# Kernel tuning notes

Hardware: AMD Instinct MI355X
Metric: run time of the kernel (lower is better)

## Reference

```python
import jax, jax.numpy as jnp
import numpy as np
from jax import lax

R = 10          # 10 iterations of (3x3x3 conv > 0) == one binary box dilation of radius 10
TOP_N = 250
SMOOTH = 1e-5
WEIGHT_CE = 1.0
WEIGHT_DICE = 1.0
FR_WEIGHT = 5.0


def _box_dilate(mask, r=R):
    # binary dilation with a (2r+1)^3 box, done separably along D,H,W
    x = mask.astype(jnp.float32)
    for axis in (1, 2, 3):
        win = [1, 1, 1, 1]
        win[axis] = 2 * r + 1
        x = lax.reduce_window(x, 0.0, lax.max, tuple(win), (1, 1, 1, 1), 'SAME')
    return x > 0


def _masked_mean(x, mask):
    cnt = jnp.sum(mask)
    s = jnp.sum(jnp.where(mask, x, 0.0))
    return jnp.where(cnt > 0, s / jnp.maximum(cnt, 1), 0.0)


def _fr_loss(feature, label):
    pos = label[:, 0] == 1                                  # (B,D,H,W)
    neg = label[:, 0] == 0
    f = jnp.moveaxis(feature, 1, -1)                        # (B,D,H,W,C)
    cnt = jnp.sum(pos)
    # mean positive feature (zeros if no positives)
    mean_pos = jnp.sum(jnp.where(pos[..., None], f, 0.0), axis=(0, 1, 2, 3)) / jnp.maximum(cnt, 1)
    std_feat = jnp.where(cnt > 0, mean_pos, 0.0)
    std_n = std_feat / jnp.maximum(jnp.linalg.norm(std_feat), 1e-12)
    # normalized feature map; cosine of a normalized feature with std_n == dot product
    f_n = f / jnp.maximum(jnp.linalg.norm(f, axis=-1, keepdims=True), 1e-12)
    cos_map = jnp.einsum('bdhwc,c->bdhw', f_n, std_n)
    # 1) positive compactness loss
    positive_loss = _masked_mean(1.0 - cos_map, pos)
    easy = _box_dilate(pos) & (~pos)
    mis_loss = _masked_mean(jax.nn.relu(cos_map), easy)
    # 3) hardest negatives: top-250 negative similarities, scatter to mask, dilate
    neg_sims = jnp.where(neg, cos_map, -1e30).reshape(-1)
    top_v, top_i = lax.top_k(neg_sims, TOP_N)
    hi = jnp.zeros(neg_sims.shape, jnp.float32).at[top_i].set((top_v > -1e29).astype(jnp.float32))
    hi = hi.reshape(pos.shape) > 0
    final_neg = _box_dilate(hi) & (~pos)
    neg_loss = _masked_mean(jax.nn.relu(cos_map), final_neg)
    return positive_loss + mis_loss + neg_loss


def _ce_and_dice(net_output, target):
    C = net_output.shape[1]
    logp = jax.nn.log_softmax(net_output, axis=1)           # (B,C,D,H,W)
    ce = -jnp.mean(jnp.take_along_axis(logp, target, axis=1))
    p = jnp.exp(logp)
    y = jax.nn.one_hot(target[:, 0], C, dtype=p.dtype)      # (B,D,H,W,C)
    y = jnp.moveaxis(y, -1, 1)                               # (B,C,D,H,W)
    axes = (0, 2, 3, 4)                                      # batch_dice=True
    tp = jnp.sum(p * y, axes)
    fp = jnp.sum(p * (1.0 - y), axes)
    fn = jnp.sum((1.0 - p) * y, axes)
    dc = (2.0 * tp + SMOOTH) / jnp.maximum(2.0 * tp + fp + fn + SMOOTH, 1e-8)
    dc_loss = -jnp.mean(dc[1:])                              # do_bg=False
    return ce, dc_loss


def setup_inputs() -> dict:
    key = jax.random.key(0)
    k1, k2, k3 = jax.random.split(key, 3)
    B, Cf, Cls, S = 2, 16, 3, 128
    feature = jax.random.normal(k1, (B, Cf, S, S, S), dtype=jnp.float32)
    net_output = jax.random.normal(k2, (B, Cls, S, S, S), dtype=jnp.float32)
    target = jax.random.randint(k3, (B, 1, S, S, S), 0, 3, dtype=jnp.int32)
    return {"feature": feature, "net_output": net_output, "target": target}


def reference(feature, net_output, target):
    ce, dc = _ce_and_dice(net_output, target)
    fr = _fr_loss(feature, target)
    return WEIGHT_CE * ce + WEIGHT_DICE * dc + FR_WEIGHT * fr
```

## Files before the change

kernel.cpp:

```cpp
#include <hip/hip_runtime.h>
#include <hip/hip_bf16.h>
#include <math.h>

#define S3    128
#define NB    2
#define CF    16
#define CHS   (S3*S3*S3)
#define NVOX  (NB*CHS)
#define NW    (NVOX/64)
#define CAP   1048576

typedef unsigned long long u64;
typedef unsigned int u32;

#define ACC_OFF    0
#define STD_OFF    512
#define SCAN_OFF   576
#define HIST_OFF   1024
#define HIB_OFF    (HIST_OFF + 4096*4)
#define ZERO_BYTES (HIB_OFF + NW*8)
#define POSB_OFF   544768
#define NEGB_OFF   (POSB_OFF + NW*8)
#define DTMP_OFF   (NEGB_OFF + NW*8)
#define DILP_OFF   (DTMP_OFF + 2*NW*8)
#define DILH_OFF   (DILP_OFF + NW*8)
#define CAND_OFF   (DILH_OFF + NW*8)
#define COS_OFF    (CAND_OFF + CAP*8)


__device__ __forceinline__ double wave_red(double x) {
    for (int o = 32; o > 0; o >>= 1) x += __shfl_down(x, o);
    return x;
}
__device__ __forceinline__ u32 mono_key(float f) {
    u32 u = __float_as_uint(f);
    return (u & 0x80000000u) ? ~u : (u | 0x80000000u);
}
__device__ __forceinline__ u64 spread4(u32 x16) {
    u64 x = (u64)(x16 & 0xFFFFu);
    x = (x | (x << 24)) & 0x000000FF000000FFull;
    x = (x | (x << 12)) & 0x000F000F000F000Full;
    x = (x | (x << 6))  & 0x0303030303030303ull;
    x = (x | (x << 3))  & 0x1111111111111111ull;
    return x;
}

template<int NBINS>
__device__ __forceinline__ void sel_desc(const u32* h, u32 need, u32* ss, u32* res)
{
    const int t = threadIdx.x;
    const int CH = NBINS / 256;
    u32 s = 0;
    #pragma unroll
    for (int j = 0; j < CH; j++) s += h[t * CH + j];
    ss[t] = s;
    __syncthreads();
    for (int o = 1; o < 256; o <<= 1) {
        u32 v = (t + o < 256) ? ss[t + o] : 0;
        __syncthreads();
        ss[t] += v;
        __syncthreads();
    }
    u32 above = ss[t] - s;
    if (above < need && above + s >= need) {
        u32 cum = above;
        int bin = t * CH;
        for (int b = t * CH + CH - 1; b >= t * CH; b--) {
            if (cum + h[b] >= need) { bin = b; break; }
            cum += h[b];
        }
        res[0] = (u32)bin;
        res[1] = need - cum;
    }
    __syncthreads();
}

__global__ __launch_bounds__(256) void k_main(const float* __restrict__ feat,
        const float* __restrict__ net, const int* __restrict__ tgt,
        u64* __restrict__ posb, u64* __restrict__ negb, double* __restrict__ acc)
{
    int tid = blockIdx.x * 256 + threadIdx.x;
    const int gstride = gridDim.x * 256;
    const int lane = threadIdx.x & 63;
    float fs[16];
    #pragma unroll
    for (int c = 0; c < 16; c++) fs[c] = 0.f;
    float ce = 0.f, s0 = 0.f, s1 = 0.f, s2 = 0.f, ta0 = 0.f, ta1 = 0.f, ta2 = 0.f;
    int n0 = 0, n1 = 0, n2 = 0;

    for (int idx = tid; idx < NVOX / 4; idx += gstride) {
        const int v4 = idx << 2;
        const int b = v4 >> 21;
        const int4 tv = *(const int4*)(tgt + v4);
        const int T[4] = {tv.x, tv.y, tv.z, tv.w};
        u32 nib_p = (u32)(T[0]==1) | ((u32)(T[1]==1)<<1) | ((u32)(T[2]==1)<<2) | ((u32)(T[3]==1)<<3);
        u32 nib_n = (u32)(T[0]==0) | ((u32)(T[1]==0)<<1) | ((u32)(T[2]==0)<<2) | ((u32)(T[3]==0)<<3);
        int pp = __popc(nib_p), nn_ = __popc(nib_n);
        n1 += pp; n0 += nn_; n2 += 4 - pp - nn_;

        u64 bp0 = __ballot(nib_p & 1), bp1 = __ballot(nib_p & 2),
            bp2 = __ballot(nib_p & 4), bp3 = __ballot(nib_p & 8);
        u64 bn0 = __ballot(nib_n & 1), bn1 = __ballot(nib_n & 2),
            bn2 = __ballot(nib_n & 4), bn3 = __ballot(nib_n & 8);
        if ((lane & 15) == 0) {
            int wsel = lane >> 4, sh = wsel << 4;
            u64 wp = spread4((u32)(bp0 >> sh)) | (spread4((u32)(bp1 >> sh)) << 1)
                   | (spread4((u32)(bp2 >> sh)) << 2) | (spread4((u32)(bp3 >> sh)) << 3);
            u64 wn = spread4((u32)(bn0 >> sh)) | (spread4((u32)(bn1 >> sh)) << 1)
                   | (spread4((u32)(bn2 >> sh)) << 2) | (spread4((u32)(bn3 >> sh)) << 3);
            int wi = ((idx - lane) >> 4) + wsel;
            posb[wi] = wp; negb[wi] = wn;
        }

        const size_t nbase = (size_t)v4 + (size_t)b * (2u * CHS);
        float4 a0 = *(const float4*)(net + nbase);
        float4 a1 = *(const float4*)(net + nbase + CHS);
        float4 a2 = *(const float4*)(net + nbase + 2 * (size_t)CHS);
        const float X0[4] = {a0.x, a0.y, a0.z, a0.w};
        const float X1[4] = {a1.x, a1.y, a1.z, a1.w};
        const float X2[4] = {a2.x, a2.y, a2.z, a2.w};
        #pragma unroll
        for (int j = 0; j < 4; j++) {
            float x0 = X0[j], x1 = X1[j], x2 = X2[j];
            float m = fmaxf(x0, fmaxf(x1, x2));
            float e0 = expf(x0 - m), e1 = expf(x1 - m), e2 = expf(x2 - m);
            float sum = e0 + e1 + e2;
            float lse = m + logf(sum);
            int t = T[j];
            float xt = (t == 0) ? x0 : ((t == 1) ? x1 : x2);
            ce += lse - xt;
            float inv = 1.f / sum;
            float p0 = e0 * inv, p1 = e1 * inv, p2 = e2 * inv;
            s0 += p0; s1 += p1; s2 += p2;
            if (t == 0) ta0 += p0; else if (t == 1) ta1 += p1; else ta2 += p2;
        }

        if (nib_p) {
            const float* fb = feat + (size_t)v4 + (size_t)b * ((size_t)(CF - 1) * CHS);
            float w0 = (float)(nib_p & 1), w1 = (float)((nib_p >> 1) & 1),
                  w2 = (float)((nib_p >> 2) & 1), w3 = (float)((nib_p >> 3) & 1);
            #pragma unroll
            for (int c = 0; c < 16; c++) {
                float4 f = *(const float4*)(fb + (size_t)c * CHS);
                fs[c] += f.x * w0 + f.y * w1 + f.z * w2 + f.w * w3;
            }
        }
    }

    __shared__ double red[4][26];
    double vals[26];
    #pragma unroll
    for (int c = 0; c < 16; c++) vals[c] = (double)fs[c];
    vals[16] = n0; vals[17] = n1; vals[18] = n2;
    vals[19] = ce; vals[20] = s0; vals[21] = s1; vals[22] = s2;
    vals[23] = ta0; vals[24] = ta1; vals[25] = ta2;
    int wid = threadIdx.x >> 6;
    #pragma unroll
    for (int i = 0; i < 26; i++) {
        double x = wave_red(vals[i]);
        if (lane == 0) red[wid][i] = x;
    }
    __syncthreads();
    if (threadIdx.x < 26) {
        double s = red[0][threadIdx.x] + red[1][threadIdx.x] + red[2][threadIdx.x] + red[3][threadIdx.x];
        atomicAdd(&acc[threadIdx.x], s);
    }
}

__global__ void k_std(const double* __restrict__ acc, float* __restrict__ stdn) {
    __shared__ float v[16];
    double cnt = acc[17];
    if (threadIdx.x < 16) {
        double mp = acc[threadIdx.x] / fmax(cnt, 1.0);
        v[threadIdx.x] = (cnt > 0.0) ? (float)mp : 0.0f;
    }
    __syncthreads();
    if (threadIdx.x == 0) {
        float n = 0;
        for (int c = 0; c < 16; c++) n += v[c] * v[c];
        n = fmaxf(sqrtf(n), 1e-12f);
        for (int c = 0; c < 16; c++) stdn[c] = v[c] / n;
    }
}

__global__ __launch_bounds__(256) void k_cos(const float* __restrict__ feat,
        const float* __restrict__ stdn, const u64* __restrict__ negb,
        float* __restrict__ cosm, u32* __restrict__ hist)
{
    __shared__ u32 h[4096];
    __shared__ float sn[16];
    for (int i = threadIdx.x; i < 4096; i += 256) h[i] = 0;
    if (threadIdx.x < 16) sn[threadIdx.x] = stdn[threadIdx.x];
    __syncthreads();
    int tid = blockIdx.x * 256 + threadIdx.x;
    const int gstride = gridDim.x * 256;
    for (int idx = tid; idx < NVOX / 4; idx += gstride) {
        const int v4 = idx << 2;
        const int b = v4 >> 21;
        const float* fb = feat + (size_t)v4 + (size_t)b * ((size_t)(CF - 1) * CHS);
        float d0 = 0, d1 = 0, d2 = 0, d3 = 0, q0 = 0, q1 = 0, q2 = 0, q3 = 0;
        #pragma unroll
        for (int c = 0; c < 16; c++) {
            float4 f = *(const float4*)(fb + (size_t)c * CHS);
            float s = sn[c];
            d0 = fmaf(f.x, s, d0); q0 = fmaf(f.x, f.x, q0);
            d1 = fmaf(f.y, s, d1); q1 = fmaf(f.y, f.y, q1);
            d2 = fmaf(f.z, s, d2); q2 = fmaf(f.z, f.z, q2);
            d3 = fmaf(f.w, s, d3); q3 = fmaf(f.w, f.w, q3);
        }
        float c0 = d0 / fmaxf(sqrtf(q0), 1e-12f);
        float c1 = d1 / fmaxf(sqrtf(q1), 1e-12f);
        float c2 = d2 / fmaxf(sqrtf(q2), 1e-12f);
        float c3 = d3 / fmaxf(sqrtf(q3), 1e-12f);
        *(float4*)(cosm + v4) = make_float4(c0, c1, c2, c3);
        u32 nib = (u32)(negb[v4 >> 6] >> (v4 & 63)) & 0xFu;
        if (nib & 1) atomicAdd(&h[mono_key(c0) >> 20], 1u);
        if (nib & 2) atomicAdd(&h[mono_key(c1) >> 20], 1u);
        if (nib & 4) atomicAdd(&h[mono_key(c2) >> 20], 1u);
        if (nib & 8) atomicAdd(&h[mono_key(c3) >> 20], 1u);
    }
    __syncthreads();
    for (int i = threadIdx.x; i < 4096; i += 256)
        if (h[i]) atomicAdd(&hist[i], h[i]);
}

__global__ __launch_bounds__(256) void k_scanA(const u32* __restrict__ hist, u32* __restrict__ scan) {
    __shared__ u32 h[4096];
    __shared__ u32 ss[256];
    __shared__ u32 res[2];
    for (int i = threadIdx.x; i < 4096; i += 256) h[i] = hist[i];
    __syncthreads();
    sel_desc<4096>(h, 250u, ss, res);
    if (threadIdx.x == 0) { scan[0] = res[0]; scan[1] = res[1]; }
}

__global__ __launch_bounds__(256) void k_collect(const float* __restrict__ cosm,
        const u64* __restrict__ negb, u32* __restrict__ scan, u64* __restrict__ cand)
{
    const u32 thr = scan[0] << 20;
    int tid = blockIdx.x * 256 + threadIdx.x;
    const int gstride = gridDim.x * 256;
    for (int idx = tid; idx < NVOX / 4; idx += gstride) {
        const int v4 = idx << 2;
        u32 nib = (u32)(negb[v4 >> 6] >> (v4 & 63)) & 0xFu;
        if (!nib) continue;
        float4 cv = *(const float4*)(cosm + v4);
        const float C[4] = {cv.x, cv.y, cv.z, cv.w};
        #pragma unroll
        for (int j = 0; j < 4; j++) {
            if ((nib >> j) & 1) {
                u32 key = mono_key(C[j]);
                if (key >= thr) {
                    u32 p = atomicAdd(&scan[4], 1u);
                    if (p < CAP) cand[p] = ((u64)key << 32) | (u32)(v4 + j);
                }
            }
        }
    }
}

__global__ __launch_bounds__(256) void k_select(const u64* __restrict__ cand,
        const u32* __restrict__ scan, u64* __restrict__ hib)
{
    __shared__ u32 h[4096];
    __shared__ u32 ss[256];
    __shared__ u32 res[2];
    __shared__ u32 eqlist[2048];
    __shared__ u32 eqc;
    const u32 cnt = scan[4];
    const int n = (int)(cnt < CAP ? cnt : CAP);
    const u32 binA = scan[0];
    const u32 need1 = scan[1];

    for (int i = threadIdx.x; i < 4096; i += 256) h[i] = 0;
    if (threadIdx.x == 0) eqc = 0;
    __syncthreads();
    for (int i = threadIdx.x; i < n; i += 256) {
        u32 key = (u32)(cand[i] >> 32);
        if ((key >> 20) == binA) atomicAdd(&h[(key >> 8) & 0xFFFu], 1u);
    }
    __syncthreads();
    sel_desc<4096>(h, need1, ss, res);
    const u32 b1 = res[0], need2 = res[1];

    for (int i = threadIdx.x; i < 4096; i += 256) h[i] = 0;
    __syncthreads();
    const u32 pre24 = (binA << 12) | b1;
    for (int i = threadIdx.x; i < n; i += 256) {
        u32 key = (u32)(cand[i] >> 32);
        if ((key >> 8) == pre24) atomicAdd(&h[key & 0xFFu], 1u);
    }
    __syncthreads();
    sel_desc<256>(h, need2, ss, res);
    const u32 K = (pre24 << 8) | res[0];
    const u32 need3 = res[1];

    for (int i = threadIdx.x; i < n; i += 256) {
        u64 code = cand[i];
        u32 key = (u32)(code >> 32), vi = (u32)code;
        if (key > K) atomicOr(&hib[vi >> 6], 1ull << (vi & 63));
        else if (key == K) { u32 p = atomicAdd(&eqc, 1u); if (p < 2048) eqlist[p] = vi; }
    }
    __syncthreads();
    if (threadIdx.x == 0) {
        int m = (int)(eqc < 2048u ? eqc : 2048u);
        u32 prev = 0; bool first = true;
        for (u32 k = 0; k < need3; k++) {
            u32 best = 0xFFFFFFFFu;
            for (int i = 0; i < m; i++) {
                u32 x = eqlist[i];
                if ((first || x > prev) && x < best) best = x;
            }
            if (best == 0xFFFFFFFFu) break;
            atomicOr(&hib[best >> 6], 1ull << (best & 63));
            prev = best; first = false;
        }
    }
}

__global__ __launch_bounds__(256) void k_dilD(const u64* __restrict__ posb,
        const u64* __restrict__ hib, u64* __restrict__ dtmp)
{
    int t = blockIdx.x * 256 + threadIdx.x;
    int m = t >> 16, wI = t & 65535;
    const u64* in = m ? hib : posb;
    int dd = (wI >> 8) & 127;
    int base = wI - (dd << 8);
    int lo = dd > 10 ? dd - 10 : 0, hi2 = dd + 10 > 127 ? 127 : dd + 10;
    u64 r = 0;
    for (int j = lo; j <= hi2; j++) r |= in[base + (j << 8)];
    dtmp[t] = r;
}

__global__ __launch_bounds__(256) void k_dilHW(const u64* __restrict__ dtmp,
        u64* __restrict__ dilp, u64* __restrict__ dilh)
{
    __shared__ u64 A[256], Bsh[256];
    int m = blockIdx.x >> 8, s = blockIdx.x & 255;
    int slicebase = (m << 16) + s * 256;
    A[threadIdx.x] = dtmp[slicebase + threadIdx.x];
    __syncthreads();
    int hh = threadIdx.x >> 1, col = threadIdx.x & 1;
    int lo = hh > 10 ? hh - 10 : 0, hi2 = hh + 10 > 127 ? 127 : hh + 10;
    u64 r = 0;
    for (int j = lo; j <= hi2; j++) r |= A[(j << 1) + col];
    Bsh[threadIdx.x] = r;
    __syncthreads();
    if (threadIdx.x < 128) {
        u64 lo64 = Bsh[threadIdx.x * 2], hi64 = Bsh[threadIdx.x * 2 + 1];
        u64 rl = lo64, rh = hi64;
        #pragma unroll
        for (int sft = 1; sft <= 10; sft++) {
            rl |= (lo64 << sft) | (lo64 >> sft) | (hi64 << (64 - sft));
            rh |= (hi64 << sft) | (hi64 >> sft) | (lo64 >> (64 - sft));
        }
        u64* out = m ? dilh : dilp;
        int wbase = s * 256 + threadIdx.x * 2;
        out[wbase] = rl; out[wbase + 1] = rh;
    }
}

__global__ __launch_bounds__(256) void k_fin(const float* __restrict__ cosm,
        const u64* __restrict__ posb, const u64* __restrict__ dilp,
        const u64* __restrict__ dilh, double* __restrict__ acc)
{
    int tid = blockIdx.x * 256 + threadIdx.x;
    const int gstride = gridDim.x * 256;
    const int lane = threadIdx.x & 63;
    float sp = 0.f, se = 0.f, sf = 0.f;
    int cE = 0, cF = 0;
    for (int idx = tid; idx < NVOX / 4; idx += gstride) {
        const int v4 = idx << 2;
        int wI = v4 >> 6, sh = v4 & 63;
        u64 pb = posb[wI];
        u32 np_ = (u32)(pb >> sh) & 0xFu;
        u32 ne  = (u32)(((dilp[wI] & ~pb) >> sh)) & 0xFu;
        u32 nf  = (u32)(((dilh[wI] & ~pb) >> sh)) & 0xFu;
        if (!(np_ | ne | nf)) continue;
        float4 cv = *(const float4*)(cosm + v4);
        const float C[4] = {cv.x, cv.y, cv.z, cv.w};
        #pragma unroll
        for (int j = 0; j < 4; j++) {
            float cs = C[j], rl = fmaxf(cs, 0.f);
            if ((np_ >> j) & 1) sp += 1.f - cs;
            if ((ne >> j) & 1) { se += rl; cE++; }
            if ((nf >> j) & 1) { sf += rl; cF++; }
        }
    }
    __shared__ double red[4][5];
    int wid = threadIdx.x >> 6;
    double vals[5] = {(double)sp, (double)se, (double)cE, (double)sf, (double)cF};
    #pragma unroll
    for (int i = 0; i < 5; i++) {
        double x = wave_red(vals[i]);
        if (lane == 0) red[wid][i] = x;
    }
    __syncthreads();
    if (threadIdx.x < 5) {
        double s = red[0][threadIdx.x] + red[1][threadIdx.x] + red[2][threadIdx.x] + red[3][threadIdx.x];
        atomicAdd(&acc[26 + threadIdx.x], s);
    }
}

__global__ void k_combine(const double* __restrict__ acc, float* __restrict__ out) {
    if (threadIdx.x != 0 || blockIdx.x != 0) return;
    double ce = acc[19] / (double)NVOX;
    double dcl = 0;
    for (int c = 1; c <= 2; c++) {
        double T = acc[23 + c], S = acc[20 + c], N = acc[16 + c];
        dcl += (2.0 * T + 1e-5) / fmax(S + N + 1e-5, 1e-8);
    }
    double dc_loss = -(dcl / 2.0);
    double cnt = acc[17];
    double pl = (cnt > 0.0) ? acc[26] / fmax(cnt, 1.0) : 0.0;
    double ml = (acc[28] > 0.0) ? acc[27] / acc[28] : 0.0;
    double nl = (acc[30] > 0.0) ? acc[29] / acc[30] : 0.0;
    out[0] = (float)(ce + dc_loss + 5.0 * (pl + ml + nl));
}

extern "C" void kernel_launch(void* const* d_in, const int* in_sizes, int n_in,
                              void* d_out, int out_size, void* d_ws, size_t ws_size,
                              hipStream_t stream)
{
    const float* feat = (const float*)d_in[0];
    const float* net  = (const float*)d_in[1];
    const int*   tgt  = (const int*)d_in[2];
    float* out = (float*)d_out;
    char* w = (char*)d_ws;

    double* acc  = (double*)(w + ACC_OFF);
    float* stdn  = (float*)(w + STD_OFF);
    u32* scan    = (u32*)(w + SCAN_OFF);
    u32* hist    = (u32*)(w + HIST_OFF);
    u64* hib     = (u64*)(w + HIB_OFF);
    u64* posb    = (u64*)(w + POSB_OFF);
    u64* negb    = (u64*)(w + NEGB_OFF);
    u64* dtmp    = (u64*)(w + DTMP_OFF);
    u64* dilp    = (u64*)(w + DILP_OFF);
    u64* dilh    = (u64*)(w + DILH_OFF);
    u64* cand    = (u64*)(w + CAND_OFF);
    float* cosm  = (float*)(w + COS_OFF);

    hipMemsetAsync(w, 0, ZERO_BYTES, stream);

    k_main   <<<2048, 256, 0, stream>>>(feat, net, tgt, posb, negb, acc);
    k_std    <<<1,    64,  0, stream>>>(acc, stdn);
    k_cos    <<<2048, 256, 0, stream>>>(feat, stdn, negb, cosm, hist);
    k_scanA  <<<1,    256, 0, stream>>>(hist, scan);
    k_collect<<<2048, 256, 0, stream>>>(cosm, negb, scan, cand);
    k_select <<<1,    256, 0, stream>>>(cand, scan, hib);
    k_dilD   <<<512,  256, 0, stream>>>(posb, hib, dtmp);
    k_dilHW  <<<512,  256, 0, stream>>>(dtmp, dilp, dilh);
    k_fin    <<<2048, 256, 0, stream>>>(cosm, posb, dilp, dilh, acc);
    k_combine<<<1,    64,  0, stream>>>(acc, out);
}
```

Measured before the change: 224.7 us.

## Fuse H/W dilation with final masked reductions and use nontemporal loads

```diff
diff --git a/kernel.cpp b/kernel.cpp
--- a/kernel.cpp
+++ b/kernel.cpp
@@ -12,6 +12,8 @@
 
 typedef unsigned long long u64;
 typedef unsigned int u32;
+typedef float f4 __attribute__((ext_vector_type(4)));
+typedef int   i4 __attribute__((ext_vector_type(4)));
 
 #define ACC_OFF    0
 #define STD_OFF    512
@@ -22,9 +24,7 @@
 #define POSB_OFF   544768
 #define NEGB_OFF   (POSB_OFF + NW*8)
 #define DTMP_OFF   (NEGB_OFF + NW*8)
-#define DILP_OFF   (DTMP_OFF + 2*NW*8)
-#define DILH_OFF   (DILP_OFF + NW*8)
-#define CAND_OFF   (DILH_OFF + NW*8)
+#define CAND_OFF   (DTMP_OFF + 2*NW*8)
 #define COS_OFF    (CAND_OFF + CAP*8)
 
 
@@ -91,8 +91,8 @@
     for (int idx = tid; idx < NVOX / 4; idx += gstride) {
         const int v4 = idx << 2;
         const int b = v4 >> 21;
-        const int4 tv = *(const int4*)(tgt + v4);
-        const int T[4] = {tv.x, tv.y, tv.z, tv.w};
+        const i4 tv = __builtin_nontemporal_load((const i4*)(tgt + v4));
+        const int T[4] = {tv[0], tv[1], tv[2], tv[3]};
         u32 nib_p = (u32)(T[0]==1) | ((u32)(T[1]==1)<<1) | ((u32)(T[2]==1)<<2) | ((u32)(T[3]==1)<<3);
         u32 nib_n = (u32)(T[0]==0) | ((u32)(T[1]==0)<<1) | ((u32)(T[2]==0)<<2) | ((u32)(T[3]==0)<<3);
         int pp = __popc(nib_p), nn_ = __popc(nib_n);
@@ -113,15 +113,12 @@
         }
 
         const size_t nbase = (size_t)v4 + (size_t)b * (2u * CHS);
-        float4 a0 = *(const float4*)(net + nbase);
-        float4 a1 = *(const float4*)(net + nbase + CHS);
-        float4 a2 = *(const float4*)(net + nbase + 2 * (size_t)CHS);
-        const float X0[4] = {a0.x, a0.y, a0.z, a0.w};
-        const float X1[4] = {a1.x, a1.y, a1.z, a1.w};
-        const float X2[4] = {a2.x, a2.y, a2.z, a2.w};
+        f4 a0 = __builtin_nontemporal_load((const f4*)(net + nbase));
+        f4 a1 = __builtin_nontemporal_load((const f4*)(net + nbase + CHS));
+        f4 a2 = __builtin_nontemporal_load((const f4*)(net + nbase + 2 * (size_t)CHS));
         #pragma unroll
         for (int j = 0; j < 4; j++) {
-            float x0 = X0[j], x1 = X1[j], x2 = X2[j];
+            float x0 = a0[j], x1 = a1[j], x2 = a2[j];
             float m = fmaxf(x0, fmaxf(x1, x2));
             float e0 = expf(x0 - m), e1 = expf(x1 - m), e2 = expf(x2 - m);
             float sum = e0 + e1 + e2;
@@ -208,16 +205,17 @@
             d2 = fmaf(f.z, s, d2); q2 = fmaf(f.z, f.z, q2);
             d3 = fmaf(f.w, s, d3); q3 = fmaf(f.w, f.w, q3);
         }
-        float c0 = d0 / fmaxf(sqrtf(q0), 1e-12f);
-        float c1 = d1 / fmaxf(sqrtf(q1), 1e-12f);
-        float c2 = d2 / fmaxf(sqrtf(q2), 1e-12f);
-        float c3 = d3 / fmaxf(sqrtf(q3), 1e-12f);
-        *(float4*)(cosm + v4) = make_float4(c0, c1, c2, c3);
+        f4 cv;
+        cv[0] = d0 / fmaxf(sqrtf(q0), 1e-12f);
+        cv[1] = d1 / fmaxf(sqrtf(q1), 1e-12f);
+        cv[2] = d2 / fmaxf(sqrtf(q2), 1e-12f);
+        cv[3] = d3 / fmaxf(sqrtf(q3), 1e-12f);
+        __builtin_nontemporal_store(cv, (f4*)(cosm + v4));
         u32 nib = (u32)(negb[v4 >> 6] >> (v4 & 63)) & 0xFu;
-        if (nib & 1) atomicAdd(&h[mono_key(c0) >> 20], 1u);
-        if (nib & 2) atomicAdd(&h[mono_key(c1) >> 20], 1u);
-        if (nib & 4) atomicAdd(&h[mono_key(c2) >> 20], 1u);
-        if (nib & 8) atomicAdd(&h[mono_key(c3) >> 20], 1u);
+        if (nib & 1) atomicAdd(&h[mono_key(cv[0]) >> 20], 1u);
+        if (nib & 2) atomicAdd(&h[mono_key(cv[1]) >> 20], 1u);
+        if (nib & 4) atomicAdd(&h[mono_key(cv[2]) >> 20], 1u);
+        if (nib & 8) atomicAdd(&h[mono_key(cv[3]) >> 20], 1u);
     }
     __syncthreads();
     for (int i = threadIdx.x; i < 4096; i += 256)
@@ -332,63 +330,64 @@
     dtmp[t] = r;
 }
 
-__global__ __launch_bounds__(256) void k_dilHW(const u64* __restrict__ dtmp,
-        u64* __restrict__ dilp, u64* __restrict__ dilh)
-{
-    __shared__ u64 A[256], Bsh[256];
-    int m = blockIdx.x >> 8, s = blockIdx.x & 255;
-    int slicebase = (m << 16) + s * 256;
-    A[threadIdx.x] = dtmp[slicebase + threadIdx.x];
-    __syncthreads();
-    int hh = threadIdx.x >> 1, col = threadIdx.x & 1;
-    int lo = hh > 10 ? hh - 10 : 0, hi2 = hh + 10 > 127 ? 127 : hh + 10;
-    u64 r = 0;
-    for (int j = lo; j <= hi2; j++) r |= A[(j << 1) + col];
-    Bsh[threadIdx.x] = r;
-    __syncthreads();
-    if (threadIdx.x < 128) {
-        u64 lo64 = Bsh[threadIdx.x * 2], hi64 = Bsh[threadIdx.x * 2 + 1];
-        u64 rl = lo64, rh = hi64;
+__global__ __launch_bounds__(256) void k_dilfin(const u64* __restrict__ dtmp,
+        const u64* __restrict__ posb, const float* __restrict__ cosm,
+        double* __restrict__ acc)
+{
+    __shared__ u64 A0[256], A1[256], B0[256], B1[256], E[256], F[256], P[256];
+    __shared__ double red[4][5];
+    const int s = blockIdx.x;
+    const int t = threadIdx.x;
+    const int sbase = s * 256;
+    A0[t] = dtmp[sbase + t];
+    A1[t] = dtmp[65536 + sbase + t];
+    P[t]  = posb[sbase + t];
+    __syncthreads();
+    {
+        int hh = t >> 1, col = t & 1;
+        int lo = hh > 10 ? hh - 10 : 0, hi2 = hh + 10 > 127 ? 127 : hh + 10;
+        u64 r0 = 0, r1 = 0;
+        for (int j = lo; j <= hi2; j++) { r0 |= A0[(j << 1) + col]; r1 |= A1[(j << 1) + col]; }
+        B0[t] = r0; B1[t] = r1;
+    }
+    __syncthreads();
+    if (t < 128) {
+        u64 lo0 = B0[t * 2], hi0 = B0[t * 2 + 1];
+        u64 lo1 = B1[t * 2], hi1 = B1[t * 2 + 1];
+        u64 rl0 = lo0, rh0 = hi0, rl1 = lo1, rh1 = hi1;
         #pragma unroll
         for (int sft = 1; sft <= 10; sft++) {
-            rl |= (lo64 << sft) | (lo64 >> sft) | (hi64 << (64 - sft));
-            rh |= (hi64 << sft) | (hi64 >> sft) | (lo64 >> (64 - sft));
-        }
-        u64* out = m ? dilh : dilp;
-        int wbase = s * 256 + threadIdx.x * 2;
-        out[wbase] = rl; out[wbase + 1] = rh;
-    }
-}
-
-__global__ __launch_bounds__(256) void k_fin(const float* __restrict__ cosm,
-        const u64* __restrict__ posb, const u64* __restrict__ dilp,
-        const u64* __restrict__ dilh, double* __restrict__ acc)
-{
-    int tid = blockIdx.x * 256 + threadIdx.x;
-    const int gstride = gridDim.x * 256;
-    const int lane = threadIdx.x & 63;
+            rl0 |= (lo0 << sft) | (lo0 >> sft) | (hi0 << (64 - sft));
+            rh0 |= (hi0 << sft) | (hi0 >> sft) | (lo0 >> (64 - sft));
+            rl1 |= (lo1 << sft) | (lo1 >> sft) | (hi1 << (64 - sft));
+            rh1 |= (hi1 << sft) | (hi1 >> sft) | (lo1 >> (64 - sft));
+        }
+        E[t * 2] = rl0; E[t * 2 + 1] = rh0;
+        F[t * 2] = rl1; F[t * 2 + 1] = rh1;
+    }
+    __syncthreads();
     float sp = 0.f, se = 0.f, sf = 0.f;
     int cE = 0, cF = 0;
-    for (int idx = tid; idx < NVOX / 4; idx += gstride) {
-        const int v4 = idx << 2;
-        int wI = v4 >> 6, sh = v4 & 63;
-        u64 pb = posb[wI];
-        u32 np_ = (u32)(pb >> sh) & 0xFu;
-        u32 ne  = (u32)(((dilp[wI] & ~pb) >> sh)) & 0xFu;
-        u32 nf  = (u32)(((dilh[wI] & ~pb) >> sh)) & 0xFu;
+    const float* cbase = cosm + (size_t)s * 16384;
+    #pragma unroll 4
+    for (int i = 0; i < 16; i++) {
+        int q = t + 256 * i;
+        int lw = q >> 4, sh = (q & 15) * 4;
+        u64 pw = P[lw];
+        u32 np_ = (u32)(pw >> sh) & 0xFu;
+        u32 ne  = (u32)((E[lw] & ~pw) >> sh) & 0xFu;
+        u32 nf  = (u32)((F[lw] & ~pw) >> sh) & 0xFu;
         if (!(np_ | ne | nf)) continue;
-        float4 cv = *(const float4*)(cosm + v4);
-        const float C[4] = {cv.x, cv.y, cv.z, cv.w};
+        f4 cv = __builtin_nontemporal_load((const f4*)(cbase + q * 4));
         #pragma unroll
         for (int j = 0; j < 4; j++) {
-            float cs = C[j], rl = fmaxf(cs, 0.f);
+            float cs = cv[j], rl = fmaxf(cs, 0.f);
             if ((np_ >> j) & 1) sp += 1.f - cs;
             if ((ne >> j) & 1) { se += rl; cE++; }
             if ((nf >> j) & 1) { sf += rl; cF++; }
         }
     }
-    __shared__ double red[4][5];
-    int wid = threadIdx.x >> 6;
+    int lane = t & 63, wid = t >> 6;
     double vals[5] = {(double)sp, (double)se, (double)cE, (double)sf, (double)cF};
     #pragma unroll
     for (int i = 0; i < 5; i++) {
@@ -396,9 +395,9 @@
         if (lane == 0) red[wid][i] = x;
     }
     __syncthreads();
-    if (threadIdx.x < 5) {
-        double s = red[0][threadIdx.x] + red[1][threadIdx.x] + red[2][threadIdx.x] + red[3][threadIdx.x];
-        atomicAdd(&acc[26 + threadIdx.x], s);
+    if (t < 5) {
+        double sum = red[0][t] + red[1][t] + red[2][t] + red[3][t];
+        atomicAdd(&acc[26 + t], sum);
     }
 }
 
@@ -436,8 +435,6 @@
     u64* posb    = (u64*)(w + POSB_OFF);
     u64* negb    = (u64*)(w + NEGB_OFF);
     u64* dtmp    = (u64*)(w + DTMP_OFF);
-    u64* dilp    = (u64*)(w + DILP_OFF);
-    u64* dilh    = (u64*)(w + DILH_OFF);
     u64* cand    = (u64*)(w + CAND_OFF);
     float* cosm  = (float*)(w + COS_OFF);
 
@@ -450,7 +447,6 @@
     k_collect<<<2048, 256, 0, stream>>>(cosm, negb, scan, cand);
     k_select <<<1,    256, 0, stream>>>(cand, scan, hib);
     k_dilD   <<<512,  256, 0, stream>>>(posb, hib, dtmp);
-    k_dilHW  <<<512,  256, 0, stream>>>(dtmp, dilp, dilh);
-    k_fin    <<<2048, 256, 0, stream>>>(cosm, posb, dilp, dilh, acc);
+    k_dilfin <<<256,  256, 0, stream>>>(dtmp, posb, cosm, acc);
     k_combine<<<1,    64,  0, stream>>>(acc, out);
 }
```

New measurement: 197.6 us. 12.0% less time.
